# Kernel tuning notes

Measured on AMD Instinct MI355X. Metric: run time of the kernel, lower is better.

## Reference

```python
import jax, jax.numpy as jnp
import numpy as np

EPS = 1e-12  # F.normalize eps

def _l2_normalize(x, axis=-1):
    n = jnp.linalg.norm(x, axis=axis, keepdims=True)
    return x / jnp.maximum(n, EPS)

def setup_inputs() -> dict:
    key = jax.random.key(0)
    ks = jax.random.split(key, 7)
    B, D, E = 16384, 512, 1024
    return {
        "query": jax.random.normal(ks[0], (B, D), dtype=jnp.float32),
        "episode_keys": jax.random.normal(ks[1], (E, D), dtype=jnp.float32),
        "episode_values": jax.random.normal(ks[2], (E, D), dtype=jnp.float32),
        "Wq": jax.random.normal(ks[3], (D, D), dtype=jnp.float32) * (1.0 / np.sqrt(D)),
        "Wv": jax.random.normal(ks[4], (D, D), dtype=jnp.float32) * (1.0 / np.sqrt(D)),
        "Wg": jax.random.normal(ks[5], (D, 2 * D), dtype=jnp.float32) * (1.0 / np.sqrt(2 * D)),
        "bg": jax.random.normal(ks[6], (D,), dtype=jnp.float32) * 0.01,
        "top_k": 4,
    }

def reference(query, episode_keys, episode_values, Wq, Wv, Wg, bg, top_k):
    # q = query_proj(query); cosine similarity against normalized episode keys
    q = query @ Wq.T                                   # [B, D]
    q_norm = _l2_normalize(q, axis=-1)                 # [B, D]
    keys_norm = _l2_normalize(episode_keys, axis=-1)   # [E, D]
    sim = q_norm @ keys_norm.T                         # [B, E]
    top_vals, top_idx = jax.lax.top_k(sim, top_k)      # [B, k]
    weights = jax.nn.softmax(top_vals * 5.0, axis=-1)  # [B, k]
    selected = jnp.take(episode_values, top_idx, axis=0)  # [B, k, D]
    retrieved = jnp.einsum('bk,bkd->bd', weights, selected)
    projected = retrieved @ Wv.T                       # [B, D]
    gate_input = jnp.concatenate([query, projected], axis=-1)  # [B, 2D]
    gate_val = jax.nn.sigmoid(gate_input @ Wg.T + bg)  # [B, D]
    return gate_val * projected
```

## Files before the change

kernel.cpp:

```cpp
#include <hip/hip_runtime.h>
#include <hip/hip_bf16.h>
#include <math.h>


#define B_ 16384
#define D_ 512
#define E_ 1024

typedef __attribute__((ext_vector_type(8))) short bf16x8;
typedef __attribute__((ext_vector_type(4))) float f32x4;
typedef __attribute__((ext_vector_type(8))) unsigned short u16x8;

__device__ __forceinline__ unsigned short f2bf(float f) {
  unsigned u = __builtin_bit_cast(unsigned, f);
  unsigned r = (u + 0x7fffu + ((u >> 16) & 1u)) >> 16;
  return (unsigned short)r;
}
__device__ __forceinline__ float bf2f(unsigned short u) {
  return __builtin_bit_cast(float, (unsigned)u << 16);
}

#define GLDS16(g, l)                                                          \
  __builtin_amdgcn_global_load_lds(                                           \
      (const __attribute__((address_space(1))) void*)(g),                     \
      (__attribute__((address_space(3))) void*)(l), 16, 0, 0)

__global__ __launch_bounds__(64) void l2norm_keys(const float* __restrict__ in,
                                                  float* __restrict__ outF,
                                                  unsigned short* __restrict__ outBF) {
  const int row  = blockIdx.x;
  const int lane = threadIdx.x;
  const float4* p4 = (const float4*)(in + (size_t)row * D_);
  float4 a = p4[lane];
  float4 b = p4[lane + 64];
  float ss = a.x*a.x + a.y*a.y + a.z*a.z + a.w*a.w
           + b.x*b.x + b.y*b.y + b.z*b.z + b.w*b.w;
#pragma unroll
  for (int off = 32; off > 0; off >>= 1) ss += __shfl_xor(ss, off, 64);
  const float inv = 1.0f / fmaxf(sqrtf(ss), 1e-12f);
  a.x *= inv; a.y *= inv; a.z *= inv; a.w *= inv;
  b.x *= inv; b.y *= inv; b.z *= inv; b.w *= inv;
  float4* o4 = (float4*)(outF + (size_t)row * D_);
  o4[lane]      = a;
  o4[lane + 64] = b;
  ushort4 ua, ub;
  ua.x=f2bf(a.x); ua.y=f2bf(a.y); ua.z=f2bf(a.z); ua.w=f2bf(a.w);
  ub.x=f2bf(b.x); ub.y=f2bf(b.y); ub.z=f2bf(b.z); ub.w=f2bf(b.w);
  *(ushort4*)(outBF + (size_t)row * D_ + 4*lane)       = ua;
  *(ushort4*)(outBF + (size_t)row * D_ + 256 + 4*lane) = ub;
}

__global__ __launch_bounds__(256) void transpose512(const float* __restrict__ in,
                                                    float* __restrict__ out) {
  __shared__ float t[32][33];
  const int tx = threadIdx.x & 31, ty = threadIdx.x >> 5;
  const int bx = blockIdx.x, by = blockIdx.y;
#pragma unroll
  for (int k = 0; k < 4; k++)
    t[ty + 8*k][tx] = in[(size_t)(by*32 + ty + 8*k) * 512 + bx*32 + tx];
  __syncthreads();
#pragma unroll
  for (int k = 0; k < 4; k++)
    out[(size_t)(bx*32 + ty + 8*k) * 512 + by*32 + tx] = t[tx][ty + 8*k];
}

__global__ __launch_bounds__(256) void sgemm64(const float* __restrict__ A,
                                               const float* __restrict__ Bm,
                                               float* __restrict__ C) {
  __shared__ float As[16][64];
  __shared__ float Bs[16][64];
  const int tid = threadIdx.x;
  const int bn = blockIdx.x, bm = blockIdx.y;
  const int tm = tid >> 4, tn = tid & 15;
  const int r = tid >> 2, k4 = (tid & 3) * 4;
  const float* Ap = A  + (size_t)(bm*64 + r) * 512 + k4;
  const float* Bp = Bm + (size_t)(bn*64 + r) * 512 + k4;
  float acc[4][4];
#pragma unroll
  for (int i = 0; i < 4; i++)
#pragma unroll
    for (int j = 0; j < 4; j++) acc[i][j] = 0.0f;

  for (int k0 = 0; k0 < 512; k0 += 16) {
    const float4 av = *(const float4*)(Ap + k0);
    const float4 bv = *(const float4*)(Bp + k0);
    As[k4+0][r]=av.x; As[k4+1][r]=av.y; As[k4+2][r]=av.z; As[k4+3][r]=av.w;
    Bs[k4+0][r]=bv.x; Bs[k4+1][r]=bv.y; Bs[k4+2][r]=bv.z; Bs[k4+3][r]=bv.w;
    __syncthreads();
#pragma unroll
    for (int k = 0; k < 16; k++) {
      const float4 a = *(const float4*)&As[k][tm*4];
      const float4 b = *(const float4*)&Bs[k][tn*4];
      const float aa[4] = {a.x,a.y,a.z,a.w}, bb[4] = {b.x,b.y,b.z,b.w};
#pragma unroll
      for (int i = 0; i < 4; i++)
#pragma unroll
        for (int j = 0; j < 4; j++) acc[i][j] = fmaf(aa[i], bb[j], acc[i][j]);
    }
    __syncthreads();
  }
#pragma unroll
  for (int i = 0; i < 4; i++) {
    float4 o = make_float4(acc[i][0], acc[i][1], acc[i][2], acc[i][3]);
    *(float4*)(C + (size_t)(bm*64 + tm*4 + i) * 512 + bn*64 + tn*4) = o;
  }
}

__global__ __launch_bounds__(256) void cvt_bf16(const float* __restrict__ in,
                                                unsigned short* __restrict__ out, int n8) {
  const int i = blockIdx.x * 256 + threadIdx.x;
  if (i >= n8) return;
  const float4 a = ((const float4*)in)[2*i];
  const float4 b = ((const float4*)in)[2*i+1];
  u16x8 o;
  o[0]=f2bf(a.x); o[1]=f2bf(a.y); o[2]=f2bf(a.z); o[3]=f2bf(a.w);
  o[4]=f2bf(b.x); o[5]=f2bf(b.y); o[6]=f2bf(b.z); o[7]=f2bf(b.w);
  *(u16x8*)(out + 8*i) = o;
}

__global__ __launch_bounds__(256) void qgemm_norm(
    const float* __restrict__ query,
    const unsigned short* __restrict__ Wqbf,
    unsigned short* __restrict__ qnbf,
    float* __restrict__ invq) {
  __shared__ __align__(16) unsigned short As[2][64 * 32];
  __shared__ __align__(16) unsigned short Bs[2][512 * 32];
  __shared__ float rowss[4][64];
  const int tid = threadIdx.x;
  const int wv = tid >> 6, l = tid & 63;
  const int m0 = blockIdx.x * 64;
  const int lane16 = l & 15, lhi = l >> 4;

  f32x4 acc[4][8];
#pragma unroll
  for (int mi = 0; mi < 4; mi++)
#pragma unroll
    for (int nj = 0; nj < 8; nj++)
#pragma unroll
      for (int r = 0; r < 4; r++) acc[mi][nj][r] = 0.0f;

  auto stage = [&](int buf, int t) {
    const int k0 = t * 32;
    {
      const int p = tid;
      const int r = p >> 2, c = p & 3;
      const int q = k0 + 8 * (c ^ ((r >> 1) & 3));
      const float* src = query + (size_t)(m0 + r) * 512 + q;
      const float4 f0 = *(const float4*)src;
      const float4 f1 = *(const float4*)(src + 4);
      u16x8 o;
      o[0]=f2bf(f0.x); o[1]=f2bf(f0.y); o[2]=f2bf(f0.z); o[3]=f2bf(f0.w);
      o[4]=f2bf(f1.x); o[5]=f2bf(f1.y); o[6]=f2bf(f1.z); o[7]=f2bf(f1.w);
      *(u16x8*)&As[buf][p * 8] = o;
    }
#pragma unroll
    for (int h = 0; h < 8; ++h) {
      const int p = tid + 256 * h;
      const int r = p >> 2, c = p & 3;
      const int q = k0 + 8 * (c ^ ((r >> 1) & 3));
      GLDS16(Wqbf + (size_t)r * 512 + q, &Bs[buf][(4 * h + wv) * 512]);
    }
  };
  auto compute = [&](int buf) {
    const int achunk = lhi ^ ((lane16 >> 1) & 3);
    bf16x8 af[4], bfr[8];
#pragma unroll
    for (int mi = 0; mi < 4; ++mi)
      af[mi] = *(const bf16x8*)&As[buf][(mi * 16 + lane16) * 32 + achunk * 8];
#pragma unroll
    for (int nj = 0; nj < 8; ++nj)
      bfr[nj] = *(const bf16x8*)&Bs[buf][(wv * 128 + nj * 16 + lane16) * 32 + achunk * 8];
#pragma unroll
    for (int mi = 0; mi < 4; ++mi)
#pragma unroll
      for (int nj = 0; nj < 8; ++nj)
        acc[mi][nj] = __builtin_amdgcn_mfma_f32_16x16x32_bf16(af[mi], bfr[nj], acc[mi][nj], 0, 0, 0);
  };

  stage(0, 0);
  __syncthreads();
  for (int t = 0; t < 15; ++t) {
    stage((t + 1) & 1, t + 1);
    compute(t & 1);
    __syncthreads();
  }
  compute(1);

  float ss[4][4];
#pragma unroll
  for (int mi = 0; mi < 4; mi++)
#pragma unroll
    for (int r = 0; r < 4; r++) ss[mi][r] = 0.0f;
#pragma unroll
  for (int mi = 0; mi < 4; mi++)
#pragma unroll
    for (int nj = 0; nj < 8; nj++)
#pragma unroll
      for (int r = 0; r < 4; r++) {
        const float x = acc[mi][nj][r];
        ss[mi][r] = fmaf(x, x, ss[mi][r]);
      }
#pragma unroll
  for (int off = 1; off < 16; off <<= 1)
#pragma unroll
    for (int mi = 0; mi < 4; mi++)
#pragma unroll
      for (int r = 0; r < 4; r++) ss[mi][r] += __shfl_xor(ss[mi][r], off, 64);
  if (lane16 == 0) {
#pragma unroll
    for (int mi = 0; mi < 4; mi++)
#pragma unroll
      for (int r = 0; r < 4; r++) rowss[wv][mi * 16 + lhi * 4 + r] = ss[mi][r];
  }
  __syncthreads();

#pragma unroll
  for (int mi = 0; mi < 4; mi++) {
#pragma unroll
    for (int r = 0; r < 4; r++) {
      const int row = mi * 16 + lhi * 4 + r;
      const float tot = rowss[0][row] + rowss[1][row] + rowss[2][row] + rowss[3][row];
      const float inv = 1.0f / fmaxf(sqrtf(tot), 1e-12f);
      if (wv == 0 && lane16 == 0) invq[m0 + row] = inv;
#pragma unroll
      for (int nj = 0; nj < 8; nj++)
        qnbf[(size_t)(m0 + row) * 512 + wv * 128 + nj * 16 + lane16] =
            f2bf(acc[mi][nj][r] * inv);
    }
  }
}

template<int KTOT, int NOUT, int MODE>
__global__ __launch_bounds__(256) void mfma_nt(
    const unsigned short* __restrict__ A0bf,
    const float* __restrict__ A0f,
    const unsigned short* __restrict__ A1,
    const unsigned short* __restrict__ Bw,
    const float* __restrict__ bg,
    const float* __restrict__ projf,
    float* __restrict__ outf,
    unsigned short* __restrict__ outbf) {
  __shared__ __align__(16) unsigned short As[2][128 * 32];
  __shared__ __align__(16) unsigned short Bs[2][128 * 32];
  const int tid = threadIdx.x;
  const int wv = tid >> 6, l = tid & 63;
  const int bn = blockIdx.x, bm = blockIdx.y;
  const int wr = wv >> 1, wc = wv & 1;
  const int lane16 = l & 15, lhi = l >> 4;

  f32x4 acc[4][4];
#pragma unroll
  for (int mi = 0; mi < 4; mi++)
#pragma unroll
    for (int nj = 0; nj < 4; nj++)
#pragma unroll
      for (int r = 0; r < 4; r++) acc[mi][nj][r] = 0.0f;

  auto stage = [&](int buf, int t) {
    const int k0 = t * 32;
#pragma unroll
    for (int h = 0; h < 2; ++h) {
      const int p = tid + 256 * h;
      const int r = p >> 2, c = p & 3;
      const int q = k0 + 8 * (c ^ ((r >> 1) & 3));
      if constexpr (MODE == 2) {
        if (k0 < 512) {
          const float* asrcF = A0f + (size_t)(bm * 128 + r) * 512 + q;
          const float4 f0 = *(const float4*)asrcF;
          const float4 f1 = *(const float4*)(asrcF + 4);
          u16x8 o;
          o[0]=f2bf(f0.x); o[1]=f2bf(f0.y); o[2]=f2bf(f0.z); o[3]=f2bf(f0.w);
          o[4]=f2bf(f1.x); o[5]=f2bf(f1.y); o[6]=f2bf(f1.z); o[7]=f2bf(f1.w);
          *(u16x8*)&As[buf][(size_t)p * 8] = o;
        } else {
          const unsigned short* asrc = A1 + (size_t)(bm * 128 + r) * 512 + (q - 512);
          GLDS16(asrc, &As[buf][(4 * h + wv) * 512]);
        }
      } else {
        const unsigned short* asrc = A0bf + (size_t)(bm * 128 + r) * 512 + q;
        GLDS16(asrc, &As[buf][(4 * h + wv) * 512]);
      }
      const unsigned short* bsrc = Bw + (size_t)(bn * 128 + r) * KTOT + q;
      GLDS16(bsrc, &Bs[buf][(4 * h + wv) * 512]);
    }
  };

  auto compute = [&](int buf) {
    const int achunk = lhi ^ ((lane16 >> 1) & 3);
    bf16x8 af[4], bfr[4];
#pragma unroll
    for (int mi = 0; mi < 4; ++mi)
      af[mi] = *(const bf16x8*)&As[buf][(wr * 64 + mi * 16 + lane16) * 32 + achunk * 8];
#pragma unroll
    for (int nj = 0; nj < 4; ++nj)
      bfr[nj] = *(const bf16x8*)&Bs[buf][(wc * 64 + nj * 16 + lane16) * 32 + achunk * 8];
#pragma unroll
    for (int mi = 0; mi < 4; ++mi)
#pragma unroll
      for (int nj = 0; nj < 4; ++nj)
        acc[mi][nj] = __builtin_amdgcn_mfma_f32_16x16x32_bf16(af[mi], bfr[nj], acc[mi][nj], 0, 0, 0);
  };

  const int NT = KTOT / 32;
  stage(0, 0);
  __syncthreads();
  for (int t = 0; t < NT - 1; ++t) {
    stage((t + 1) & 1, t + 1);
    compute(t & 1);
    __syncthreads();
  }
  compute((NT - 1) & 1);

  const int rowb = bm * 128 + wr * 64 + (lhi << 2);
  const int colb = bn * 128 + wc * 64 + lane16;
#pragma unroll
  for (int mi = 0; mi < 4; ++mi) {
#pragma unroll
    for (int nj = 0; nj < 4; ++nj) {
      const int col = colb + nj * 16;
#pragma unroll
      for (int r = 0; r < 4; ++r) {
        const int row = rowb + mi * 16 + r;
        const size_t o = (size_t)row * NOUT + col;
        const float v = acc[mi][nj][r];
        if constexpr (MODE == 2) {
          const float x = v + bg[col];
          const float g = 1.0f / (1.0f + __expf(-x));
          outf[o] = g * projf[o];
        } else if constexpr (MODE == 1) {
          outf[o]  = v;
          outbf[o] = f2bf(v);
        } else {
          outbf[o] = f2bf(v);
        }
      }
    }
  }
}

__global__ __launch_bounds__(256) void topk_rescore_gather(
    const unsigned short* __restrict__ simbf,
    const float* __restrict__ query,
    const float* __restrict__ invq,
    const float* __restrict__ Kp,
    const float* __restrict__ vals,
    unsigned short* __restrict__ retr) {
  const int w = threadIdx.x >> 6, l = threadIdx.x & 63;
  const int b = blockIdx.x * 4 + w;
  const float NEG = -3.402823466e38f;
  __shared__ float qT[4][512];
  __shared__ int   s_idx[4][16];
  __shared__ int   s_cnt[4];
  __shared__ int   s_fr[64];
  __shared__ int   s_fi[64];
  __shared__ float s_fs[64];

  const float4* qp = (const float4*)(query + (size_t)b * D_ + 8 * l);
  const float4 qa = qp[0], qb = qp[1];
  qT[w][0*64+l]=qa.x; qT[w][1*64+l]=qa.y; qT[w][2*64+l]=qa.z; qT[w][3*64+l]=qa.w;
  qT[w][4*64+l]=qb.x; qT[w][5*64+l]=qb.y; qT[w][6*64+l]=qb.z; qT[w][7*64+l]=qb.w;

  const u16x8* sp = (const u16x8*)(simbf + (size_t)b * E_ + 16 * l);
  const u16x8 s0 = sp[0], s1 = sp[1];
  float v[16];
#pragma unroll
  for (int j = 0; j < 8; j++) {
    v[j]     = bf2f((unsigned short)s0[j]);
    v[8 + j] = bf2f((unsigned short)s1[j]);
  }

  unsigned killed = 0;
  float t4 = NEG;
  int c0 = 0, c1 = 0, c2 = 0, c3 = 0;
#pragma unroll
  for (int k = 0; k < 4; k++) {
    float bv = NEG; int bs = 0;
#pragma unroll
    for (int j = 0; j < 16; j++) {
      const float vj = ((killed >> j) & 1u) ? NEG : v[j];
      if (vj > bv) { bv = vj; bs = j; }
    }
    int bi = l * 16 + bs;
#pragma unroll
    for (int off = 32; off > 0; off >>= 1) {
      const float ov = __shfl_xor(bv, off, 64);
      const int   oi = __shfl_xor(bi, off, 64);
      if (ov > bv || (ov == bv && oi < bi)) { bv = ov; bi = oi; }
    }
    if ((bi >> 4) == l) killed |= 1u << (bi & 15);
    if (k == 0) c0 = bi; else if (k == 1) c1 = bi; else if (k == 2) c2 = bi; else c3 = bi;
    t4 = bv;
  }
  if (l == 0) { s_idx[w][0]=c0; s_idx[w][1]=c1; s_idx[w][2]=c2; s_idx[w][3]=c3; }

  int cnt = 4;
  const float thr = t4 - 0.008f;
#pragma unroll
  for (int s = 0; s < 16; s++) {
    const bool pred = (((killed >> s) & 1u) == 0u) && (v[s] >= thr);
    unsigned long long m = __ballot(pred);
    while (m) {
      const int ln = __builtin_ctzll(m);
      m &= m - 1;
      if (cnt < 16) { if (l == 0) s_idx[w][cnt] = ln * 16 + s; }
      cnt++;
    }
  }
  if (cnt > 16) cnt = 16;
  if (l == 0) s_cnt[w] = cnt;
  __syncthreads();

  const int n0 = s_cnt[0], n1 = s_cnt[1], n2 = s_cnt[2], n3 = s_cnt[3];
  const int tot = n0 + n1 + n2 + n3;
  const int off = (w > 0 ? n0 : 0) + (w > 1 ? n1 : 0) + (w > 2 ? n2 : 0);
  if (l < s_cnt[w]) { s_fr[off + l] = w; s_fi[off + l] = s_idx[w][l]; }
  __syncthreads();

  for (int g = w; g < tot; g += 4) {
    const int r   = s_fr[g];
    const int idx = s_fi[g];
    const float4* kp = (const float4*)(Kp + (size_t)idx * D_ + 8 * l);
    const float4 k0 = kp[0], k1 = kp[1];
    float p =        qT[r][0*64+l] * k0.x;
    p = fmaf(qT[r][1*64+l], k0.y, p);
    p = fmaf(qT[r][2*64+l], k0.z, p);
    p = fmaf(qT[r][3*64+l], k0.w, p);
    p = fmaf(qT[r][4*64+l], k1.x, p);
    p = fmaf(qT[r][5*64+l], k1.y, p);
    p = fmaf(qT[r][6*64+l], k1.z, p);
    p = fmaf(qT[r][7*64+l], k1.w, p);
#pragma unroll
    for (int o = 32; o > 0; o >>= 1) p += __shfl_xor(p, o, 64);
    if (l == 0) s_fs[g] = p;
  }
  __syncthreads();

  float rv0 = NEG, rv1 = NEG, rv2 = NEG, rv3 = NEG;
  int   ri0 = 0x7fffffff, ri1 = 0x7fffffff, ri2 = 0x7fffffff, ri3 = 0x7fffffff;
  auto ins = [&](float nv, int ni) {
    if (nv > rv0 || (nv == rv0 && ni < ri0)) {
      rv3 = rv2; ri3 = ri2; rv2 = rv1; ri2 = ri1; rv1 = rv0; ri1 = ri0; rv0 = nv; ri0 = ni;
    } else if (nv > rv1 || (nv == rv1 && ni < ri1)) {
      rv3 = rv2; ri3 = ri2; rv2 = rv1; ri2 = ri1; rv1 = nv; ri1 = ni;
    } else if (nv > rv2 || (nv == rv2 && ni < ri2)) {
      rv3 = rv2; ri3 = ri2; rv2 = nv; ri2 = ni;
    } else if (nv > rv3 || (nv == rv3 && ni < ri3)) {
      rv3 = nv; ri3 = ni;
    }
  };
  const int mycnt = s_cnt[w];
  for (int j = 0; j < mycnt; j++) ins(s_fs[off + j], s_fi[off + j]);

  const float iq = invq[b];
  const float f0 = rv0 * iq, f1 = rv1 * iq, f2 = rv2 * iq, f3 = rv3 * iq;
  const float mx = 5.0f * f0;
  const float e0 = expf(5.0f * f0 - mx), e1 = expf(5.0f * f1 - mx);
  const float e2 = expf(5.0f * f2 - mx), e3 = expf(5.0f * f3 - mx);
  const float wi = 1.0f / (e0 + e1 + e2 + e3);
  const float w0 = e0 * wi, w1 = e1 * wi, w2 = e2 * wi, w3 = e3 * wi;

  const float4* v0p = (const float4*)(vals + (size_t)ri0 * D_ + 8 * l);
  const float4* v1p = (const float4*)(vals + (size_t)ri1 * D_ + 8 * l);
  const float4* v2p = (const float4*)(vals + (size_t)ri2 * D_ + 8 * l);
  const float4* v3p = (const float4*)(vals + (size_t)ri3 * D_ + 8 * l);
  const float4 a0 = v0p[0], b0 = v0p[1];
  const float4 a1 = v1p[0], b1 = v1p[1];
  const float4 a2 = v2p[0], b2 = v2p[1];
  const float4 a3 = v3p[0], b3 = v3p[1];
  u16x8 o;
  o[0] = f2bf(w0 * a0.x + w1 * a1.x + w2 * a2.x + w3 * a3.x);
  o[1] = f2bf(w0 * a0.y + w1 * a1.y + w2 * a2.y + w3 * a3.y);
  o[2] = f2bf(w0 * a0.z + w1 * a1.z + w2 * a2.z + w3 * a3.z);
  o[3] = f2bf(w0 * a0.w + w1 * a1.w + w2 * a2.w + w3 * a3.w);
  o[4] = f2bf(w0 * b0.x + w1 * b1.x + w2 * b2.x + w3 * b3.x);
  o[5] = f2bf(w0 * b0.y + w1 * b1.y + w2 * b2.y + w3 * b3.y);
  o[6] = f2bf(w0 * b0.z + w1 * b1.z + w2 * b2.z + w3 * b3.z);
  o[7] = f2bf(w0 * b0.w + w1 * b1.w + w2 * b2.w + w3 * b3.w);
  *(u16x8*)(retr + (size_t)b * D_ + 8 * l) = o;
}

extern "C" void kernel_launch(void* const* d_in, const int* in_sizes, int n_in,
                              void* d_out, int out_size, void* d_ws, size_t ws_size,
                              hipStream_t stream) {
  (void)in_sizes; (void)n_in; (void)out_size; (void)ws_size;
  const float* query = (const float*)d_in[0];
  const float* keys  = (const float*)d_in[1];
  const float* vals  = (const float*)d_in[2];
  const float* Wq    = (const float*)d_in[3];
  const float* Wv    = (const float*)d_in[4];
  const float* Wg    = (const float*)d_in[5];
  const float* bg    = (const float*)d_in[6];
  float* out = (float*)d_out;

  char* ws = (char*)d_ws;
  const size_t M = 1u << 20;
  unsigned short* sim_bf  = (unsigned short*)(ws);
  float*          projF   = (float*)(ws);
  unsigned short* qn_bf   = (unsigned short*)(ws + 32*M);
  unsigned short* retr_bf = (unsigned short*)(ws + 32*M);
  unsigned short* proj_bf = (unsigned short*)(ws + 48*M);
  float*          keysN   = (float*)(ws + 64*M);
  unsigned short* kn_bf   = (unsigned short*)(ws + 66*M);
  float*          WqT     = (float*)(ws + 67*M);
  float*          Kp      = (float*)(ws + 68*M);
  unsigned short* Wq_bf   = (unsigned short*)(ws + 70*M);
  unsigned short* Wv_bf   = (unsigned short*)(ws + 70*M + 512*1024u);
  unsigned short* Wg_bf   = (unsigned short*)(ws + 71*M);
  float*          invq    = (float*)(ws + 72*M);

  l2norm_keys<<<E_, 64, 0, stream>>>(keys, keysN, kn_bf);
  transpose512<<<dim3(16, 16), 256, 0, stream>>>(Wq, WqT);
  cvt_bf16<<<(D_ * D_ / 8 + 255) / 256, 256, 0, stream>>>(Wq, Wq_bf, D_ * D_ / 8);
  cvt_bf16<<<(D_ * D_ / 8 + 255) / 256, 256, 0, stream>>>(Wv, Wv_bf, D_ * D_ / 8);
  cvt_bf16<<<(D_ * 2 * D_ / 8 + 255) / 256, 256, 0, stream>>>(Wg, Wg_bf, D_ * 2 * D_ / 8);

  sgemm64<<<dim3(8, 16), 256, 0, stream>>>(keysN, WqT, Kp);

  qgemm_norm<<<B_ / 64, 256, 0, stream>>>(query, Wq_bf, qn_bf, invq);

  mfma_nt<512, 1024, 0><<<dim3(E_ / 128, B_ / 128), 256, 0, stream>>>(
      qn_bf, nullptr, nullptr, kn_bf, nullptr, nullptr, nullptr, sim_bf);

  topk_rescore_gather<<<B_ / 4, 256, 0, stream>>>(sim_bf, query, invq, Kp, vals, retr_bf);

  mfma_nt<512, 512, 1><<<dim3(D_ / 128, B_ / 128), 256, 0, stream>>>(
      retr_bf, nullptr, nullptr, Wv_bf, nullptr, nullptr, projF, proj_bf);

  mfma_nt<1024, 512, 2><<<dim3(D_ / 128, B_ / 128), 256, 0, stream>>>(
      nullptr, query, proj_bf, Wg_bf, bg, projF, out, nullptr);
}
```

Before: 235.4 us.

## Rework top-k selection with packed-key merge and cache bf16 query for gate GEMM

The query projection kernel now also writes a bf16 copy of the query, so the gate GEMM loads both halves of its A operand with async global-to-LDS loads instead of converting fp32 in registers. The Wv GEMM stops writing an fp32 projection; the gate epilogue reads the bf16 projection instead, which cuts memory traffic but lowers the precision of the multiplier. The top-k kernel replaces four iterative wave argmax passes and shared-memory candidate staging with a packed 32-bit key/index per-lane top-4 and a butterfly merge. Rescoring now happens directly in registers without block syncs.

```diff
diff --git a/kernel.cpp b/kernel.cpp
--- a/kernel.cpp
+++ b/kernel.cpp
@@ -122,6 +122,7 @@
     const float* __restrict__ query,
     const unsigned short* __restrict__ Wqbf,
     unsigned short* __restrict__ qnbf,
+    unsigned short* __restrict__ qbf,
     float* __restrict__ invq) {
   __shared__ __align__(16) unsigned short As[2][64 * 32];
   __shared__ __align__(16) unsigned short Bs[2][512 * 32];
@@ -152,6 +153,7 @@
       o[0]=f2bf(f0.x); o[1]=f2bf(f0.y); o[2]=f2bf(f0.z); o[3]=f2bf(f0.w);
       o[4]=f2bf(f1.x); o[5]=f2bf(f1.y); o[6]=f2bf(f1.z); o[7]=f2bf(f1.w);
       *(u16x8*)&As[buf][p * 8] = o;
+      *(u16x8*)(qbf + (size_t)(m0 + r) * 512 + q) = o;
     }
 #pragma unroll
     for (int h = 0; h < 8; ++h) {
@@ -233,11 +235,10 @@
 template<int KTOT, int NOUT, int MODE>
 __global__ __launch_bounds__(256) void mfma_nt(
     const unsigned short* __restrict__ A0bf,
-    const float* __restrict__ A0f,
     const unsigned short* __restrict__ A1,
     const unsigned short* __restrict__ Bw,
     const float* __restrict__ bg,
-    const float* __restrict__ projf,
+    const unsigned short* __restrict__ projbf,
     float* __restrict__ outf,
     unsigned short* __restrict__ outbf) {
   __shared__ __align__(16) unsigned short As[2][128 * 32];
@@ -263,23 +264,14 @@
       const int p = tid + 256 * h;
       const int r = p >> 2, c = p & 3;
       const int q = k0 + 8 * (c ^ ((r >> 1) & 3));
+      const unsigned short* asrc;
       if constexpr (MODE == 2) {
-        if (k0 < 512) {
-          const float* asrcF = A0f + (size_t)(bm * 128 + r) * 512 + q;
-          const float4 f0 = *(const float4*)asrcF;
-          const float4 f1 = *(const float4*)(asrcF + 4);
-          u16x8 o;
-          o[0]=f2bf(f0.x); o[1]=f2bf(f0.y); o[2]=f2bf(f0.z); o[3]=f2bf(f0.w);
-          o[4]=f2bf(f1.x); o[5]=f2bf(f1.y); o[6]=f2bf(f1.z); o[7]=f2bf(f1.w);
-          *(u16x8*)&As[buf][(size_t)p * 8] = o;
-        } else {
-          const unsigned short* asrc = A1 + (size_t)(bm * 128 + r) * 512 + (q - 512);
-          GLDS16(asrc, &As[buf][(4 * h + wv) * 512]);
-        }
+        asrc = (q < 512) ? (A0bf + (size_t)(bm * 128 + r) * 512 + q)
+                         : (A1   + (size_t)(bm * 128 + r) * 512 + (q - 512));
       } else {
-        const unsigned short* asrc = A0bf + (size_t)(bm * 128 + r) * 512 + q;
-        GLDS16(asrc, &As[buf][(4 * h + wv) * 512]);
+        asrc = A0bf + (size_t)(bm * 128 + r) * 512 + q;
       }
+      GLDS16(asrc, &As[buf][(4 * h + wv) * 512]);
       const unsigned short* bsrc = Bw + (size_t)(bn * 128 + r) * KTOT + q;
       GLDS16(bsrc, &Bs[buf][(4 * h + wv) * 512]);
     }
@@ -326,10 +318,7 @@
         if constexpr (MODE == 2) {
           const float x = v + bg[col];
           const float g = 1.0f / (1.0f + __expf(-x));
-          outf[o] = g * projf[o];
-        } else if constexpr (MODE == 1) {
-          outf[o]  = v;
-          outbf[o] = f2bf(v);
+          outf[o] = g * bf2f(projbf[o]);
         } else {
           outbf[o] = f2bf(v);
         }
@@ -347,94 +336,83 @@
     unsigned short* __restrict__ retr) {
   const int w = threadIdx.x >> 6, l = threadIdx.x & 63;
   const int b = blockIdx.x * 4 + w;
-  const float NEG = -3.402823466e38f;
-  __shared__ float qT[4][512];
-  __shared__ int   s_idx[4][16];
-  __shared__ int   s_cnt[4];
-  __shared__ int   s_fr[64];
-  __shared__ int   s_fi[64];
-  __shared__ float s_fs[64];
-
-  const float4* qp = (const float4*)(query + (size_t)b * D_ + 8 * l);
-  const float4 qa = qp[0], qb = qp[1];
-  qT[w][0*64+l]=qa.x; qT[w][1*64+l]=qa.y; qT[w][2*64+l]=qa.z; qT[w][3*64+l]=qa.w;
-  qT[w][4*64+l]=qb.x; qT[w][5*64+l]=qb.y; qT[w][6*64+l]=qb.z; qT[w][7*64+l]=qb.w;
 
   const u16x8* sp = (const u16x8*)(simbf + (size_t)b * E_ + 16 * l);
   const u16x8 s0 = sp[0], s1 = sp[1];
+  const float4* qp = (const float4*)(query + (size_t)b * D_ + 8 * l);
+  const float4 q0 = qp[0], q1 = qp[1];
+
   float v[16];
+  unsigned pk[16];
 #pragma unroll
   for (int j = 0; j < 8; j++) {
-    v[j]     = bf2f((unsigned short)s0[j]);
-    v[8 + j] = bf2f((unsigned short)s1[j]);
-  }
-
-  unsigned killed = 0;
-  float t4 = NEG;
-  int c0 = 0, c1 = 0, c2 = 0, c3 = 0;
-#pragma unroll
-  for (int k = 0; k < 4; k++) {
-    float bv = NEG; int bs = 0;
-#pragma unroll
-    for (int j = 0; j < 16; j++) {
-      const float vj = ((killed >> j) & 1u) ? NEG : v[j];
-      if (vj > bv) { bv = vj; bs = j; }
-    }
-    int bi = l * 16 + bs;
-#pragma unroll
-    for (int off = 32; off > 0; off >>= 1) {
-      const float ov = __shfl_xor(bv, off, 64);
-      const int   oi = __shfl_xor(bi, off, 64);
-      if (ov > bv || (ov == bv && oi < bi)) { bv = ov; bi = oi; }
-    }
-    if ((bi >> 4) == l) killed |= 1u << (bi & 15);
-    if (k == 0) c0 = bi; else if (k == 1) c1 = bi; else if (k == 2) c2 = bi; else c3 = bi;
-    t4 = bv;
-  }
-  if (l == 0) { s_idx[w][0]=c0; s_idx[w][1]=c1; s_idx[w][2]=c2; s_idx[w][3]=c3; }
-
-  int cnt = 4;
-  const float thr = t4 - 0.008f;
-#pragma unroll
-  for (int s = 0; s < 16; s++) {
-    const bool pred = (((killed >> s) & 1u) == 0u) && (v[s] >= thr);
-    unsigned long long m = __ballot(pred);
-    while (m) {
-      const int ln = __builtin_ctzll(m);
-      m &= m - 1;
-      if (cnt < 16) { if (l == 0) s_idx[w][cnt] = ln * 16 + s; }
-      cnt++;
-    }
-  }
-  if (cnt > 16) cnt = 16;
-  if (l == 0) s_cnt[w] = cnt;
-  __syncthreads();
-
-  const int n0 = s_cnt[0], n1 = s_cnt[1], n2 = s_cnt[2], n3 = s_cnt[3];
-  const int tot = n0 + n1 + n2 + n3;
-  const int off = (w > 0 ? n0 : 0) + (w > 1 ? n1 : 0) + (w > 2 ? n2 : 0);
-  if (l < s_cnt[w]) { s_fr[off + l] = w; s_fi[off + l] = s_idx[w][l]; }
-  __syncthreads();
-
-  for (int g = w; g < tot; g += 4) {
-    const int r   = s_fr[g];
-    const int idx = s_fi[g];
-    const float4* kp = (const float4*)(Kp + (size_t)idx * D_ + 8 * l);
-    const float4 k0 = kp[0], k1 = kp[1];
-    float p =        qT[r][0*64+l] * k0.x;
-    p = fmaf(qT[r][1*64+l], k0.y, p);
-    p = fmaf(qT[r][2*64+l], k0.z, p);
-    p = fmaf(qT[r][3*64+l], k0.w, p);
-    p = fmaf(qT[r][4*64+l], k1.x, p);
-    p = fmaf(qT[r][5*64+l], k1.y, p);
-    p = fmaf(qT[r][6*64+l], k1.z, p);
-    p = fmaf(qT[r][7*64+l], k1.w, p);
-#pragma unroll
-    for (int o = 32; o > 0; o >>= 1) p += __shfl_xor(p, o, 64);
-    if (l == 0) s_fs[g] = p;
-  }
-  __syncthreads();
-
+    const unsigned u0 = (unsigned short)s0[j];
+    const unsigned u1 = (unsigned short)s1[j];
+    v[j]     = bf2f((unsigned short)u0);
+    v[8 + j] = bf2f((unsigned short)u1);
+    const unsigned k0 = u0 ^ ((u0 & 0x8000u) ? 0xFFFFu : 0x8000u);
+    const unsigned k1 = u1 ^ ((u1 & 0x8000u) ? 0xFFFFu : 0x8000u);
+    pk[j]     = (k0 << 16) | (1023u - (unsigned)(l * 16 + j));
+    pk[8 + j] = (k1 << 16) | (1023u - (unsigned)(l * 16 + 8 + j));
+  }
+
+  unsigned t0 = 0, t1 = 0, t2 = 0, t3 = 0;
+#pragma unroll
+  for (int j = 0; j < 16; j++) {
+    const unsigned x = pk[j];
+    const unsigned a = min(t0, x); t0 = max(t0, x);
+    const unsigned c = min(t1, a); t1 = max(t1, a);
+    const unsigned d = min(t2, c); t2 = max(t2, c);
+    t3 = max(t3, d);
+  }
+
+#pragma unroll
+  for (int off = 1; off < 64; off <<= 1) {
+    const unsigned b0 = (unsigned)__shfl_xor((int)t0, off, 64);
+    const unsigned b1 = (unsigned)__shfl_xor((int)t1, off, 64);
+    const unsigned b2 = (unsigned)__shfl_xor((int)t2, off, 64);
+    const unsigned b3 = (unsigned)__shfl_xor((int)t3, off, 64);
+    const unsigned c0 = max(t0, b3), c1 = max(t1, b2);
+    const unsigned c2 = max(t2, b1), c3 = max(t3, b0);
+    const unsigned d0 = max(c0, c2), d2 = min(c0, c2);
+    const unsigned d1 = max(c1, c3), d3 = min(c1, c3);
+    t0 = max(d0, d1); t1 = min(d0, d1);
+    t2 = max(d2, d3); t3 = min(d2, d3);
+  }
+
+  const int i0 = 1023 - (int)(t0 & 1023u);
+  const int i1 = 1023 - (int)(t1 & 1023u);
+  const int i2 = 1023 - (int)(t2 & 1023u);
+  const int i3 = 1023 - (int)(t3 & 1023u);
+  const unsigned k16 = t3 >> 16;
+  const unsigned u4 = (k16 & 0x8000u) ? (k16 ^ 0x8000u) : (~k16 & 0xFFFFu);
+  const float thr = bf2f((unsigned short)u4) - 0.008f;
+
+  const float4* kp0 = (const float4*)(Kp + (size_t)i0 * D_ + 8 * l);
+  const float4* kp1 = (const float4*)(Kp + (size_t)i1 * D_ + 8 * l);
+  const float4* kp2 = (const float4*)(Kp + (size_t)i2 * D_ + 8 * l);
+  const float4* kp3 = (const float4*)(Kp + (size_t)i3 * D_ + 8 * l);
+  const float4 a0 = kp0[0], c0 = kp0[1];
+  const float4 a1 = kp1[0], c1 = kp1[1];
+  const float4 a2 = kp2[0], c2 = kp2[1];
+  const float4 a3 = kp3[0], c3 = kp3[1];
+  float p0 = q0.x*a0.x, p1 = q0.x*a1.x, p2 = q0.x*a2.x, p3 = q0.x*a3.x;
+  p0=fmaf(q0.y,a0.y,p0); p1=fmaf(q0.y,a1.y,p1); p2=fmaf(q0.y,a2.y,p2); p3=fmaf(q0.y,a3.y,p3);
+  p0=fmaf(q0.z,a0.z,p0); p1=fmaf(q0.z,a1.z,p1); p2=fmaf(q0.z,a2.z,p2); p3=fmaf(q0.z,a3.z,p3);
+  p0=fmaf(q0.w,a0.w,p0); p1=fmaf(q0.w,a1.w,p1); p2=fmaf(q0.w,a2.w,p2); p3=fmaf(q0.w,a3.w,p3);
+  p0=fmaf(q1.x,c0.x,p0); p1=fmaf(q1.x,c1.x,p1); p2=fmaf(q1.x,c2.x,p2); p3=fmaf(q1.x,c3.x,p3);
+  p0=fmaf(q1.y,c0.y,p0); p1=fmaf(q1.y,c1.y,p1); p2=fmaf(q1.y,c2.y,p2); p3=fmaf(q1.y,c3.y,p3);
+  p0=fmaf(q1.z,c0.z,p0); p1=fmaf(q1.z,c1.z,p1); p2=fmaf(q1.z,c2.z,p2); p3=fmaf(q1.z,c3.z,p3);
+  p0=fmaf(q1.w,c0.w,p0); p1=fmaf(q1.w,c1.w,p1); p2=fmaf(q1.w,c2.w,p2); p3=fmaf(q1.w,c3.w,p3);
+#pragma unroll
+  for (int off = 32; off > 0; off >>= 1) {
+    p0 += __shfl_xor(p0, off, 64);
+    p1 += __shfl_xor(p1, off, 64);
+    p2 += __shfl_xor(p2, off, 64);
+    p3 += __shfl_xor(p3, off, 64);
+  }
+
+  const float NEG = -3.402823466e38f;
   float rv0 = NEG, rv1 = NEG, rv2 = NEG, rv3 = NEG;
   int   ri0 = 0x7fffffff, ri1 = 0x7fffffff, ri2 = 0x7fffffff, ri3 = 0x7fffffff;
   auto ins = [&](float nv, int ni) {
@@ -448,8 +426,31 @@
       rv3 = nv; ri3 = ni;
     }
   };
-  const int mycnt = s_cnt[w];
-  for (int j = 0; j < mycnt; j++) ins(s_fs[off + j], s_fi[off + j]);
+  ins(p0, i0); ins(p1, i1); ins(p2, i2); ins(p3, i3);
+
+  auto score = [&](int idx) -> float {
+    const float4* kp = (const float4*)(Kp + (size_t)idx * D_ + 8 * l);
+    const float4 k0 = kp[0], k1 = kp[1];
+    float p = q0.x * k0.x;
+    p = fmaf(q0.y, k0.y, p); p = fmaf(q0.z, k0.z, p); p = fmaf(q0.w, k0.w, p);
+    p = fmaf(q1.x, k1.x, p); p = fmaf(q1.y, k1.y, p);
+    p = fmaf(q1.z, k1.z, p); p = fmaf(q1.w, k1.w, p);
+#pragma unroll
+    for (int off = 32; off > 0; off >>= 1) p += __shfl_xor(p, off, 64);
+    return p;
+  };
+#pragma unroll
+  for (int s = 0; s < 16; s++) {
+    const int idx = l * 16 + s;
+    const bool pred = (v[s] >= thr) && idx != i0 && idx != i1 && idx != i2 && idx != i3;
+    unsigned long long m = __ballot(pred);
+    while (m) {
+      const int ln = __builtin_ctzll(m);
+      m &= m - 1;
+      const int ci = ln * 16 + s;
+      ins(score(ci), ci);
+    }
+  }
 
   const float iq = invq[b];
   const float f0 = rv0 * iq, f1 = rv1 * iq, f2 = rv2 * iq, f3 = rv3 * iq;
@@ -463,19 +464,19 @@
   const float4* v1p = (const float4*)(vals + (size_t)ri1 * D_ + 8 * l);
   const float4* v2p = (const float4*)(vals + (size_t)ri2 * D_ + 8 * l);
   const float4* v3p = (const float4*)(vals + (size_t)ri3 * D_ + 8 * l);
-  const float4 a0 = v0p[0], b0 = v0p[1];
-  const float4 a1 = v1p[0], b1 = v1p[1];
-  const float4 a2 = v2p[0], b2 = v2p[1];
-  const float4 a3 = v3p[0], b3 = v3p[1];
+  const float4 g0 = v0p[0], h0 = v0p[1];
+  const float4 g1 = v1p[0], h1 = v1p[1];
+  const float4 g2 = v2p[0], h2 = v2p[1];
+  const float4 g3 = v3p[0], h3 = v3p[1];
   u16x8 o;
-  o[0] = f2bf(w0 * a0.x + w1 * a1.x + w2 * a2.x + w3 * a3.x);
-  o[1] = f2bf(w0 * a0.y + w1 * a1.y + w2 * a2.y + w3 * a3.y);
-  o[2] = f2bf(w0 * a0.z + w1 * a1.z + w2 * a2.z + w3 * a3.z);
-  o[3] = f2bf(w0 * a0.w + w1 * a1.w + w2 * a2.w + w3 * a3.w);
-  o[4] = f2bf(w0 * b0.x + w1 * b1.x + w2 * b2.x + w3 * b3.x);
-  o[5] = f2bf(w0 * b0.y + w1 * b1.y + w2 * b2.y + w3 * b3.y);
-  o[6] = f2bf(w0 * b0.z + w1 * b1.z + w2 * b2.z + w3 * b3.z);
-  o[7] = f2bf(w0 * b0.w + w1 * b1.w + w2 * b2.w + w3 * b3.w);
+  o[0] = f2bf(w0 * g0.x + w1 * g1.x + w2 * g2.x + w3 * g3.x);
+  o[1] = f2bf(w0 * g0.y + w1 * g1.y + w2 * g2.y + w3 * g3.y);
+  o[2] = f2bf(w0 * g0.z + w1 * g1.z + w2 * g2.z + w3 * g3.z);
+  o[3] = f2bf(w0 * g0.w + w1 * g1.w + w2 * g2.w + w3 * g3.w);
+  o[4] = f2bf(w0 * h0.x + w1 * h1.x + w2 * h2.x + w3 * h3.x);
+  o[5] = f2bf(w0 * h0.y + w1 * h1.y + w2 * h2.y + w3 * h3.y);
+  o[6] = f2bf(w0 * h0.z + w1 * h1.z + w2 * h2.z + w3 * h3.z);
+  o[7] = f2bf(w0 * h0.w + w1 * h1.w + w2 * h2.w + w3 * h3.w);
   *(u16x8*)(retr + (size_t)b * D_ + 8 * l) = o;
 }
 
@@ -494,19 +495,19 @@
 
   char* ws = (char*)d_ws;
   const size_t M = 1u << 20;
-  unsigned short* sim_bf  = (unsigned short*)(ws);
-  float*          projF   = (float*)(ws);
-  unsigned short* qn_bf   = (unsigned short*)(ws + 32*M);
-  unsigned short* retr_bf = (unsigned short*)(ws + 32*M);
-  unsigned short* proj_bf = (unsigned short*)(ws + 48*M);
-  float*          keysN   = (float*)(ws + 64*M);
-  unsigned short* kn_bf   = (unsigned short*)(ws + 66*M);
-  float*          WqT     = (float*)(ws + 67*M);
-  float*          Kp      = (float*)(ws + 68*M);
-  unsigned short* Wq_bf   = (unsigned short*)(ws + 70*M);
-  unsigned short* Wv_bf   = (unsigned short*)(ws + 70*M + 512*1024u);
-  unsigned short* Wg_bf   = (unsigned short*)(ws + 71*M);
-  float*          invq    = (float*)(ws + 72*M);
+  unsigned short* sim_bf   = (unsigned short*)(ws);
+  unsigned short* qn_bf    = (unsigned short*)(ws + 32*M);
+  unsigned short* retr_bf  = (unsigned short*)(ws + 32*M);
+  unsigned short* proj_bf  = (unsigned short*)(ws + 48*M);
+  float*          keysN    = (float*)(ws + 64*M);
+  unsigned short* kn_bf    = (unsigned short*)(ws + 66*M);
+  float*          WqT      = (float*)(ws + 67*M);
+  float*          Kp       = (float*)(ws + 68*M);
+  unsigned short* Wq_bf    = (unsigned short*)(ws + 70*M);
+  unsigned short* Wv_bf    = (unsigned short*)(ws + 70*M + 512*1024u);
+  unsigned short* Wg_bf    = (unsigned short*)(ws + 71*M);
+  float*          invq     = (float*)(ws + 72*M);
+  unsigned short* query_bf = (unsigned short*)(ws + 74*M);
 
   l2norm_keys<<<E_, 64, 0, stream>>>(keys, keysN, kn_bf);
   transpose512<<<dim3(16, 16), 256, 0, stream>>>(Wq, WqT);
@@ -516,16 +517,16 @@
 
   sgemm64<<<dim3(8, 16), 256, 0, stream>>>(keysN, WqT, Kp);
 
-  qgemm_norm<<<B_ / 64, 256, 0, stream>>>(query, Wq_bf, qn_bf, invq);
+  qgemm_norm<<<B_ / 64, 256, 0, stream>>>(query, Wq_bf, qn_bf, query_bf, invq);
 
   mfma_nt<512, 1024, 0><<<dim3(E_ / 128, B_ / 128), 256, 0, stream>>>(
-      qn_bf, nullptr, nullptr, kn_bf, nullptr, nullptr, nullptr, sim_bf);
+      qn_bf, nullptr, kn_bf, nullptr, nullptr, nullptr, sim_bf);
 
   topk_rescore_gather<<<B_ / 4, 256, 0, stream>>>(sim_bf, query, invq, Kp, vals, retr_bf);
 
-  mfma_nt<512, 512, 1><<<dim3(D_ / 128, B_ / 128), 256, 0, stream>>>(
-      retr_bf, nullptr, nullptr, Wv_bf, nullptr, nullptr, projF, proj_bf);
+  mfma_nt<512, 512, 0><<<dim3(D_ / 128, B_ / 128), 256, 0, stream>>>(
+      retr_bf, nullptr, Wv_bf, nullptr, nullptr, nullptr, proj_bf);
 
   mfma_nt<1024, 512, 2><<<dim3(D_ / 128, B_ / 128), 256, 0, stream>>>(
-      nullptr, query, proj_bf, Wg_bf, bg, projF, out, nullptr);
-}
+      query_bf, proj_bf, Wg_bf, bg, proj_bf, out, nullptr);
+}
```

Result: faster. 225.2 us (-4.3%).
